# Kernel tuning notes

Hardware: AMD Instinct MI355X
Metric: run time of the kernel (lower is better)

Reference implementation:

```python
import jax, jax.numpy as jnp
import numpy as np

B, V, E, D_IN, D_OUT = 8, 10000, 160000, 128, 128
BN_EPS = 1e-5


def setup_inputs() -> dict:
    key = jax.random.key(0)
    ks = jax.random.split(key, 8)
    X = jax.random.normal(ks[0], (B, V, D_IN), dtype=jnp.float32)
    edge_attr = jax.random.normal(ks[1], (B, E), dtype=jnp.float32)
    W_node = jax.random.normal(ks[2], (D_OUT, D_IN), dtype=jnp.float32) * (1.0 / np.sqrt(D_IN))
    W_edge = jax.random.normal(ks[3], (D_OUT, 1), dtype=jnp.float32)
    W_self = jax.random.normal(ks[4], (D_OUT, D_IN), dtype=jnp.float32) * (1.0 / np.sqrt(D_IN))
    b_self = jax.random.normal(ks[5], (D_OUT,), dtype=jnp.float32) * 0.01
    gamma = jnp.ones((D_OUT,), dtype=jnp.float32)
    beta = jnp.zeros((D_OUT,), dtype=jnp.float32)
    edge_index = jax.random.randint(ks[6], (E, 2), 0, V, dtype=jnp.int32)
    return {"X": X, "edge_attr": edge_attr, "W_node": W_node, "W_edge": W_edge,
            "W_self": W_self, "b_self": b_self, "gamma": gamma, "beta": beta,
            "edge_index": edge_index}


def reference(X, edge_attr, W_node, W_edge, W_self, b_self, gamma, beta, edge_index):
    src = edge_index[:, 0]  # [E]
    dst = edge_index[:, 1]  # [E]
    # self-loop linear
    H = jnp.einsum('bvf,of->bvo', X, W_self) + b_self  # [B,V,D_OUT]
    # fused gather -> per-edge message -> scatter-add
    msg = jnp.einsum('bef,of->beo', X[:, src, :], W_node)  # [B,E,D_OUT]
    msg = msg + edge_attr[:, :, None] * W_edge[:, 0][None, None, :]
    aggregated = jnp.zeros_like(H).at[:, dst, :].add(msg)
    H = H + aggregated
    # BatchNorm1d over channel dim (training mode, biased variance over B*V)
    mean = jnp.mean(H, axis=(0, 1))
    var = jnp.var(H, axis=(0, 1))
    Hn = (H - mean) * jax.lax.rsqrt(var + BN_EPS) * gamma + beta
    return jax.nn.relu(Hn)
```

## Files before the change

### kernel.cpp

```cpp
#include <hip/hip_runtime.h>

#define B_ 8
#define V_ 10000
#define E_ 160000
#define DIN 128
#define DOUT 128
#define M_ (B_*V_)
#define NINV (1.0f/80000.0f)
#define BN_EPS 1e-5f

#define GEMM_BLOCKS 625

#define WS_COUNTS  0
#define WS_SUM     10000
#define WS_SUMSQ   10128
#define WS_ROWPTR  10512
#define WS_CURSOR  20513
#define WS_SSRC    30513
#define WS_EAS     190520
#define WS_S       1470520
#define WS_WPK     1550520
#define WS_XH      1566904
#define WS_AH      6686904
#define WS_PART    11806904
#define WS_ZERO_UNITS 10000

typedef __attribute__((ext_vector_type(2))) _Float16 half2_t;
typedef __attribute__((ext_vector_type(4))) _Float16 half4_t;
typedef __attribute__((ext_vector_type(8))) _Float16 half8_t;
typedef __attribute__((ext_vector_type(4))) float f32x4;

__device__ inline half2_t i2h(unsigned i) {
    half2_t h; __builtin_memcpy(&h, &i, 4); return h;
}
__device__ inline unsigned h2i(half2_t h) {
    unsigned i; __builtin_memcpy(&i, &h, 4); return i;
}

__global__ __launch_bounds__(256) void prep_kernel(
    const float* __restrict__ X, _Float16* __restrict__ Xh,
    const float* __restrict__ Wself, const float* __restrict__ Wnode,
    _Float16* __restrict__ Wpk,
    const int* __restrict__ EI, int* __restrict__ counts)
{
    const int blk = blockIdx.x;
    const int t = threadIdx.x;
    if (blk < 10000) {
        int idx = blk * 256 + t;
        float4 v = ((const float4*)X)[idx];
        half4_t o = { (_Float16)v.x, (_Float16)v.y, (_Float16)v.z, (_Float16)v.w };
        ((half4_t*)Xh)[idx] = o;
    } else if (blk < 10016) {
        int g = (blk - 10000) * 256 + t;
        int pair = g >> 6;
        int lane = g & 63;
        int ks = pair >> 3;
        int nt = pair & 7;
        int o = nt * 16 + (lane & 15);
        int k = ks * 32 + (lane >> 4) * 8;
        const float* wsrc = (k < 128) ? (Wself + o * 128 + k)
                                      : (Wnode + o * 128 + (k - 128));
        _Float16* dst = Wpk + ((size_t)pair * 64 + lane) * 8;
#pragma unroll
        for (int j = 0; j < 8; ++j) dst[j] = (_Float16)wsrc[j];
    } else {
        int e = (blk - 10016) * 256 + t;
        if (e < E_) atomicAdd(&counts[EI[2 * e + 1]], 1);
    }
}

__global__ __launch_bounds__(256) void scan_kernel(
    const int* __restrict__ counts, int* __restrict__ row_ptr,
    int* __restrict__ cursor)
{
    __shared__ int psum[256];
    const int t = threadIdx.x;
    const int base = t * 40;
    int local[40];
    int s = 0;
#pragma unroll
    for (int i = 0; i < 40; ++i) {
        int idx = base + i;
        int c = (idx < V_) ? counts[idx] : 0;
        local[i] = s;
        s += c;
    }
    psum[t] = s;
    __syncthreads();
    for (int off = 1; off < 256; off <<= 1) {
        int v = (t >= off) ? psum[t - off] : 0;
        __syncthreads();
        psum[t] += v;
        __syncthreads();
    }
    int excl = (t == 0) ? 0 : psum[t - 1];
#pragma unroll
    for (int i = 0; i < 40; ++i) {
        int idx = base + i;
        if (idx < V_) {
            int rp = excl + local[i];
            row_ptr[idx] = rp;
            cursor[idx] = rp;
        }
    }
    if (t == 255) row_ptr[V_] = psum[255];
}

__global__ __launch_bounds__(256) void bucket_kernel(
    const int* __restrict__ EI, const float* __restrict__ EA,
    int* __restrict__ cursor, int* __restrict__ ssrc,
    float* __restrict__ EAs)
{
    int e = blockIdx.x * 256 + threadIdx.x;
    if (e < E_) {
        int src = EI[2 * e];
        int dst = EI[2 * e + 1];
        int p = atomicAdd(&cursor[dst], 1);
        ssrc[p] = src;
        float4 v0, v1;
        v0.x = EA[0 * E_ + e]; v0.y = EA[1 * E_ + e];
        v0.z = EA[2 * E_ + e]; v0.w = EA[3 * E_ + e];
        v1.x = EA[4 * E_ + e]; v1.y = EA[5 * E_ + e];
        v1.z = EA[6 * E_ + e]; v1.w = EA[7 * E_ + e];
        *(float4*)(EAs + (size_t)p * 8) = v0;
        *(float4*)(EAs + (size_t)p * 8 + 4) = v1;
    }
}

__global__ __launch_bounds__(256) void gather_kernel(
    const _Float16* __restrict__ Xh, const float* __restrict__ EAs,
    const int* __restrict__ row_ptr, const int* __restrict__ ssrc,
    _Float16* __restrict__ Ah, float* __restrict__ S)
{
    const int b = blockIdx.x & 7;
    const int dblk = blockIdx.x >> 3;
    const int w = threadIdx.x >> 6;
    const int lane = threadIdx.x & 63;
    const int half = lane >> 5;
    const int sl = lane & 31;
    const int d = dblk * 4 + w;
    const int wid = b * V_ + d;
    const int k0 = row_ptr[d];
    const int k1 = row_ptr[d + 1];
    const _Float16* Xb = Xh + (size_t)b * V_ * DIN + sl * 4;
    half2_t a0 = (half2_t)0, a1 = (half2_t)0;
    float ea = 0.0f;
    for (int kb = k0; kb < k1; kb += 64) {
        int cnt = min(64, k1 - kb);
        int msrc = 0;
        if (lane < cnt) {
            msrc = ssrc[kb + lane];
            ea += EAs[(size_t)(kb + lane) * 8 + b];
        }
        int j = 0;
        for (; j + 8 <= cnt; j += 8) {
#pragma unroll
            for (int u = 0; u < 4; ++u) {
                int s = __shfl(msrc, j + u * 2 + half);
                uint2 v = *(const uint2*)(Xb + (size_t)s * DIN);
                a0 += i2h(v.x);
                a1 += i2h(v.y);
            }
        }
        for (; j + 2 <= cnt; j += 2) {
            int s = __shfl(msrc, j + half);
            uint2 v = *(const uint2*)(Xb + (size_t)s * DIN);
            a0 += i2h(v.x);
            a1 += i2h(v.y);
        }
        if (j < cnt) {
            int s = __shfl(msrc, j);
            if (half == 0) {
                uint2 v = *(const uint2*)(Xb + (size_t)s * DIN);
                a0 += i2h(v.x);
                a1 += i2h(v.y);
            }
        }
    }
    unsigned c0 = __shfl_down(h2i(a0), 32);
    unsigned c1 = __shfl_down(h2i(a1), 32);
    a0 += i2h(c0);
    a1 += i2h(c1);
    for (int off = 32; off; off >>= 1) ea += __shfl_down(ea, off);
    if (lane == 0) S[wid] = ea;
    if (half == 0) {
        uint2 o;
        o.x = h2i(a0);
        o.y = h2i(a1);
        *(uint2*)(Ah + (size_t)wid * DIN + sl * 4) = o;
    }
}

__global__ __launch_bounds__(256) void mfma_gemm_kernel(
    const _Float16* __restrict__ Xh, const _Float16* __restrict__ Ah,
    const _Float16* __restrict__ Wpk, const float* __restrict__ S,
    const float* __restrict__ bself, const float* __restrict__ wedge,
    float* __restrict__ H, float* __restrict__ Partials)
{
    __shared__ float cs[128];
    __shared__ float css[128];
    const int t = threadIdx.x;
    const int wave = t >> 6;
    const int lane = t & 63;
    const int quad = lane >> 4;
    const int ln = lane & 15;
    const int rowbase = blockIdx.x * 128 + wave * 32;
    const int m0 = rowbase + ln;
    const int m1 = rowbase + 16 + ln;

    if (t < 128) { cs[t] = 0.0f; css[t] = 0.0f; }

    f32x4 acc[2][8];
#pragma unroll
    for (int mt = 0; mt < 2; ++mt)
#pragma unroll
        for (int nt = 0; nt < 8; ++nt) acc[mt][nt] = (f32x4){0.f, 0.f, 0.f, 0.f};

    const _Float16* X0 = Xh + (size_t)m0 * DIN + quad * 8;
    const _Float16* X1 = Xh + (size_t)m1 * DIN + quad * 8;
    const _Float16* A0 = Ah + (size_t)m0 * DIN + quad * 8;
    const _Float16* A1 = Ah + (size_t)m1 * DIN + quad * 8;
    const _Float16* Wl = Wpk + lane * 8;

#pragma unroll
    for (int ks = 0; ks < 8; ++ks) {
        half8_t af0, af1;
        if (ks < 4) {
            af0 = *(const half8_t*)(X0 + ks * 32);
            af1 = *(const half8_t*)(X1 + ks * 32);
        } else {
            af0 = *(const half8_t*)(A0 + (ks - 4) * 32);
            af1 = *(const half8_t*)(A1 + (ks - 4) * 32);
        }
#pragma unroll
        for (int nt = 0; nt < 8; ++nt) {
            half8_t bfr = *(const half8_t*)(Wl + (size_t)(ks * 8 + nt) * 512);
            acc[0][nt] = __builtin_amdgcn_mfma_f32_16x16x32_f16(af0, bfr, acc[0][nt], 0, 0, 0);
            acc[1][nt] = __builtin_amdgcn_mfma_f32_16x16x32_f16(af1, bfr, acc[1][nt], 0, 0, 0);
        }
    }

    float bs[8], we[8];
#pragma unroll
    for (int nt = 0; nt < 8; ++nt) {
        int c = nt * 16 + ln;
        bs[nt] = bself[c];
        we[nt] = wedge[c];
    }
    float psum[8], psq[8];
#pragma unroll
    for (int nt = 0; nt < 8; ++nt) { psum[nt] = 0.0f; psq[nt] = 0.0f; }

#pragma unroll
    for (int mt = 0; mt < 2; ++mt) {
        const int rbase = rowbase + mt * 16 + quad * 4;
        float sv[4];
#pragma unroll
        for (int r = 0; r < 4; ++r) sv[r] = S[rbase + r];
#pragma unroll
        for (int r = 0; r < 4; ++r) {
            float* Hr = H + (size_t)(rbase + r) * DOUT + ln;
#pragma unroll
            for (int nt = 0; nt < 8; ++nt) {
                float h = acc[mt][nt][r] + bs[nt] + sv[r] * we[nt];
                Hr[nt * 16] = h;
                psum[nt] += h;
                psq[nt] += h * h;
            }
        }
    }
#pragma unroll
    for (int nt = 0; nt < 8; ++nt) {
        psum[nt] += __shfl_down(psum[nt], 32);
        psum[nt] += __shfl_down(psum[nt], 16);
        psq[nt] += __shfl_down(psq[nt], 32);
        psq[nt] += __shfl_down(psq[nt], 16);
    }
    __syncthreads();
    if (lane < 16) {
#pragma unroll
        for (int nt = 0; nt < 8; ++nt) {
            atomicAdd(&cs[nt * 16 + ln], psum[nt]);
            atomicAdd(&css[nt * 16 + ln], psq[nt]);
        }
    }
    __syncthreads();
    Partials[(size_t)blockIdx.x * 256 + t] = (t < 128) ? cs[t] : css[t - 128];
}

__global__ __launch_bounds__(64) void reduce_stats_kernel(
    const float* __restrict__ Partials, float* __restrict__ gsum,
    float* __restrict__ gsumsq)
{
    const int c = blockIdx.x;
    const int t = threadIdx.x;
    float acc = 0.0f;
    for (int p = t; p < GEMM_BLOCKS; p += 64)
        acc += Partials[(size_t)p * 256 + c];
    for (int off = 32; off; off >>= 1) acc += __shfl_down(acc, off);
    if (t == 0) {
        if (c < 128) gsum[c] = acc;
        else gsumsq[c - 128] = acc;
    }
}

__global__ __launch_bounds__(256) void norm_relu_kernel(
    float* __restrict__ H, const float* __restrict__ gsum,
    const float* __restrict__ gsumsq, const float* __restrict__ gamma,
    const float* __restrict__ beta)
{
    int idx = blockIdx.x * 256 + threadIdx.x;
    int o4 = (idx & 31) * 4;
    float4 s = *(const float4*)(gsum + o4);
    float4 q = *(const float4*)(gsumsq + o4);
    float4 g = *(const float4*)(gamma + o4);
    float4 bt = *(const float4*)(beta + o4);
    float4 sc, sh;
    {
        float m0 = s.x * NINV, m1 = s.y * NINV, m2 = s.z * NINV, m3 = s.w * NINV;
        float r0 = rsqrtf(q.x * NINV - m0 * m0 + BN_EPS);
        float r1 = rsqrtf(q.y * NINV - m1 * m1 + BN_EPS);
        float r2 = rsqrtf(q.z * NINV - m2 * m2 + BN_EPS);
        float r3 = rsqrtf(q.w * NINV - m3 * m3 + BN_EPS);
        sc.x = g.x * r0; sc.y = g.y * r1; sc.z = g.z * r2; sc.w = g.w * r3;
        sh.x = bt.x - m0 * sc.x; sh.y = bt.y - m1 * sc.y;
        sh.z = bt.z - m2 * sc.z; sh.w = bt.w - m3 * sc.w;
    }
    float4 h = ((const float4*)H)[idx];
    h.x = fmaxf(h.x * sc.x + sh.x, 0.0f);
    h.y = fmaxf(h.y * sc.y + sh.y, 0.0f);
    h.z = fmaxf(h.z * sc.z + sh.z, 0.0f);
    h.w = fmaxf(h.w * sc.w + sh.w, 0.0f);
    ((float4*)H)[idx] = h;
}

extern "C" void kernel_launch(void* const* d_in, const int* in_sizes, int n_in,
                              void* d_out, int out_size, void* d_ws, size_t ws_size,
                              hipStream_t stream)
{
    const float* X      = (const float*)d_in[0];
    const float* EA     = (const float*)d_in[1];
    const float* Wnode  = (const float*)d_in[2];
    const float* Wedge  = (const float*)d_in[3];
    const float* Wself  = (const float*)d_in[4];
    const float* bself  = (const float*)d_in[5];
    const float* gamma  = (const float*)d_in[6];
    const float* beta   = (const float*)d_in[7];
    const int*   EI     = (const int*)d_in[8];

    int*   wsI    = (int*)d_ws;
    float* wsF    = (float*)d_ws;
    int*   counts = wsI + WS_COUNTS;
    float* gsum   = wsF + WS_SUM;
    float* gsumsq = wsF + WS_SUMSQ;
    int*   rowptr = wsI + WS_ROWPTR;
    int*   cursor = wsI + WS_CURSOR;
    int*   ssrc   = wsI + WS_SSRC;
    float* EAs    = wsF + WS_EAS;
    float* S      = wsF + WS_S;
    _Float16* Wpk = (_Float16*)(wsI + WS_WPK);
    _Float16* Xh  = (_Float16*)(wsI + WS_XH);
    _Float16* Ah  = (_Float16*)(wsI + WS_AH);
    float* Partials = wsF + WS_PART;
    float* H      = (float*)d_out;

    hipMemsetAsync(d_ws, 0, (size_t)WS_ZERO_UNITS * 4, stream);

    prep_kernel<<<10641, 256, 0, stream>>>(X, Xh, Wself, Wnode, Wpk, EI, counts);
    scan_kernel<<<1, 256, 0, stream>>>(counts, rowptr, cursor);
    bucket_kernel<<<(E_ + 255) / 256, 256, 0, stream>>>(EI, EA, cursor, ssrc, EAs);

    gather_kernel<<<M_ / 4, 256, 0, stream>>>(Xh, EAs, rowptr, ssrc, Ah, S);

    mfma_gemm_kernel<<<GEMM_BLOCKS, 256, 0, stream>>>(Xh, Ah, Wpk, S, bself,
                                                      Wedge, H, Partials);

    reduce_stats_kernel<<<256, 64, 0, stream>>>(Partials, gsum, gsumsq);

    norm_relu_kernel<<<(M_ * DOUT / 4) / 256, 256, 0, stream>>>(H, gsum, gsumsq,
                                                                gamma, beta);
}
```

Measured before the change: 226.3 us.

## Fuse GEMM, BN stats reduction and norm-ReLU into cooperative kernel; widen gather loads

```diff
diff --git a/kernel.cpp b/kernel.cpp
--- a/kernel.cpp
+++ b/kernel.cpp
@@ -1,4 +1,7 @@
 #include <hip/hip_runtime.h>
+#include <hip/hip_cooperative_groups.h>
+
+namespace cg = cooperative_groups;
 
 #define B_ 8
 #define V_ 10000
@@ -136,14 +139,14 @@
     const int dblk = blockIdx.x >> 3;
     const int w = threadIdx.x >> 6;
     const int lane = threadIdx.x & 63;
-    const int half = lane >> 5;
-    const int sl = lane & 31;
+    const int q = lane >> 4;
+    const int sl = lane & 15;
     const int d = dblk * 4 + w;
     const int wid = b * V_ + d;
     const int k0 = row_ptr[d];
     const int k1 = row_ptr[d + 1];
-    const _Float16* Xb = Xh + (size_t)b * V_ * DIN + sl * 4;
-    half2_t a0 = (half2_t)0, a1 = (half2_t)0;
+    const _Float16* Xb = Xh + (size_t)b * V_ * DIN + sl * 8;
+    half2_t a0 = (half2_t)0, a1 = (half2_t)0, a2 = (half2_t)0, a3 = (half2_t)0;
     float ea = 0.0f;
     for (int kb = k0; kb < k1; kb += 64) {
         int cnt = min(64, k1 - kb);
@@ -153,64 +156,59 @@
             ea += EAs[(size_t)(kb + lane) * 8 + b];
         }
         int j = 0;
-        for (; j + 8 <= cnt; j += 8) {
+        for (; j + 16 <= cnt; j += 16) {
 #pragma unroll
             for (int u = 0; u < 4; ++u) {
-                int s = __shfl(msrc, j + u * 2 + half);
-                uint2 v = *(const uint2*)(Xb + (size_t)s * DIN);
-                a0 += i2h(v.x);
-                a1 += i2h(v.y);
+                int s = __shfl(msrc, j + u * 4 + q);
+                uint4 v = *(const uint4*)(Xb + (size_t)s * DIN);
+                a0 += i2h(v.x); a1 += i2h(v.y); a2 += i2h(v.z); a3 += i2h(v.w);
             }
         }
-        for (; j + 2 <= cnt; j += 2) {
-            int s = __shfl(msrc, j + half);
-            uint2 v = *(const uint2*)(Xb + (size_t)s * DIN);
-            a0 += i2h(v.x);
-            a1 += i2h(v.y);
+        for (; j + 4 <= cnt; j += 4) {
+            int s = __shfl(msrc, j + q);
+            uint4 v = *(const uint4*)(Xb + (size_t)s * DIN);
+            a0 += i2h(v.x); a1 += i2h(v.y); a2 += i2h(v.z); a3 += i2h(v.w);
         }
         if (j < cnt) {
-            int s = __shfl(msrc, j);
-            if (half == 0) {
-                uint2 v = *(const uint2*)(Xb + (size_t)s * DIN);
-                a0 += i2h(v.x);
-                a1 += i2h(v.y);
+            int s = __shfl(msrc, j + q);
+            if (j + q < cnt) {
+                uint4 v = *(const uint4*)(Xb + (size_t)s * DIN);
+                a0 += i2h(v.x); a1 += i2h(v.y); a2 += i2h(v.z); a3 += i2h(v.w);
             }
         }
     }
-    unsigned c0 = __shfl_down(h2i(a0), 32);
-    unsigned c1 = __shfl_down(h2i(a1), 32);
-    a0 += i2h(c0);
-    a1 += i2h(c1);
+#pragma unroll
+    for (int off = 32; off >= 16; off >>= 1) {
+        a0 += i2h(__shfl_down(h2i(a0), off));
+        a1 += i2h(__shfl_down(h2i(a1), off));
+        a2 += i2h(__shfl_down(h2i(a2), off));
+        a3 += i2h(__shfl_down(h2i(a3), off));
+    }
     for (int off = 32; off; off >>= 1) ea += __shfl_down(ea, off);
     if (lane == 0) S[wid] = ea;
-    if (half == 0) {
-        uint2 o;
-        o.x = h2i(a0);
-        o.y = h2i(a1);
-        *(uint2*)(Ah + (size_t)wid * DIN + sl * 4) = o;
-    }
-}
-
-__global__ __launch_bounds__(256) void mfma_gemm_kernel(
+    if (lane < 16) {
+        uint4 o;
+        o.x = h2i(a0); o.y = h2i(a1); o.z = h2i(a2); o.w = h2i(a3);
+        *(uint4*)(Ah + (size_t)wid * DIN + sl * 8) = o;
+    }
+}
+
+__device__ __forceinline__ void gemm_body(
     const _Float16* __restrict__ Xh, const _Float16* __restrict__ Ah,
     const _Float16* __restrict__ Wpk, const float* __restrict__ S,
     const float* __restrict__ bself, const float* __restrict__ wedge,
-    float* __restrict__ H, float* __restrict__ Partials)
-{
-    __shared__ float cs[128];
-    __shared__ float css[128];
-    const int t = threadIdx.x;
+    int bid, int t, f32x4 (&acc)[2][8], float* cs, float* css)
+{
     const int wave = t >> 6;
     const int lane = t & 63;
     const int quad = lane >> 4;
     const int ln = lane & 15;
-    const int rowbase = blockIdx.x * 128 + wave * 32;
+    const int rowbase = bid * 128 + wave * 32;
     const int m0 = rowbase + ln;
     const int m1 = rowbase + 16 + ln;
 
     if (t < 128) { cs[t] = 0.0f; css[t] = 0.0f; }
 
-    f32x4 acc[2][8];
 #pragma unroll
     for (int mt = 0; mt < 2; ++mt)
 #pragma unroll
@@ -258,12 +256,11 @@
 #pragma unroll
         for (int r = 0; r < 4; ++r) sv[r] = S[rbase + r];
 #pragma unroll
-        for (int r = 0; r < 4; ++r) {
-            float* Hr = H + (size_t)(rbase + r) * DOUT + ln;
-#pragma unroll
-            for (int nt = 0; nt < 8; ++nt) {
+        for (int nt = 0; nt < 8; ++nt) {
+#pragma unroll
+            for (int r = 0; r < 4; ++r) {
                 float h = acc[mt][nt][r] + bs[nt] + sv[r] * we[nt];
-                Hr[nt * 16] = h;
+                acc[mt][nt][r] = h;
                 psum[nt] += h;
                 psq[nt] += h * h;
             }
@@ -285,6 +282,99 @@
         }
     }
     __syncthreads();
+}
+
+__global__ __launch_bounds__(256, 4) void gemm_norm_coop_kernel(
+    const _Float16* __restrict__ Xh, const _Float16* __restrict__ Ah,
+    const _Float16* __restrict__ Wpk, const float* __restrict__ S,
+    const float* __restrict__ bself, const float* __restrict__ wedge,
+    const float* __restrict__ gamma, const float* __restrict__ beta,
+    float* __restrict__ H, float* __restrict__ Partials,
+    float* __restrict__ gsum, float* __restrict__ gsumsq)
+{
+    __shared__ float cs[128];
+    __shared__ float css[128];
+    const int t = threadIdx.x;
+    f32x4 acc[2][8];
+    gemm_body(Xh, Ah, Wpk, S, bself, wedge, blockIdx.x, t, acc, cs, css);
+
+    Partials[(size_t)blockIdx.x * 256 + t] = (t < 128) ? cs[t] : css[t - 128];
+    __threadfence();
+    cg::this_grid().sync();
+
+    if (blockIdx.x < 256 && t < 64) {
+        const int c = blockIdx.x;
+        float a = 0.0f;
+        for (int p = t; p < GEMM_BLOCKS; p += 64)
+            a += Partials[(size_t)p * 256 + c];
+        for (int off = 32; off; off >>= 1) a += __shfl_down(a, off);
+        if (t == 0) {
+            if (c < 128) gsum[c] = a;
+            else gsumsq[c - 128] = a;
+        }
+        __threadfence();
+    }
+    cg::this_grid().sync();
+
+    const int wave = t >> 6;
+    const int lane = t & 63;
+    const int quad = lane >> 4;
+    const int ln = lane & 15;
+    const int rowbase = blockIdx.x * 128 + wave * 32;
+    float scl[8], shf[8];
+#pragma unroll
+    for (int nt = 0; nt < 8; ++nt) {
+        int c = nt * 16 + ln;
+        float gs = __hip_atomic_load(&gsum[c], __ATOMIC_RELAXED,
+                                     __HIP_MEMORY_SCOPE_AGENT);
+        float gq = __hip_atomic_load(&gsumsq[c], __ATOMIC_RELAXED,
+                                     __HIP_MEMORY_SCOPE_AGENT);
+        float mean = gs * NINV;
+        float rstd = rsqrtf(gq * NINV - mean * mean + BN_EPS);
+        scl[nt] = gamma[c] * rstd;
+        shf[nt] = beta[c] - mean * scl[nt];
+    }
+#pragma unroll
+    for (int mt = 0; mt < 2; ++mt) {
+        const int rbase = rowbase + mt * 16 + quad * 4;
+#pragma unroll
+        for (int r = 0; r < 4; ++r) {
+            float* Hr = H + (size_t)(rbase + r) * DOUT + ln;
+#pragma unroll
+            for (int nt = 0; nt < 8; ++nt)
+                Hr[nt * 16] = fmaxf(acc[mt][nt][r] * scl[nt] + shf[nt], 0.0f);
+        }
+    }
+}
+
+__global__ __launch_bounds__(256) void mfma_gemm_kernel(
+    const _Float16* __restrict__ Xh, const _Float16* __restrict__ Ah,
+    const _Float16* __restrict__ Wpk, const float* __restrict__ S,
+    const float* __restrict__ bself, const float* __restrict__ wedge,
+    float* __restrict__ H, float* __restrict__ Partials)
+{
+    __shared__ float cs[128];
+    __shared__ float css[128];
+    const int t = threadIdx.x;
+    f32x4 acc[2][8];
+    gemm_body(Xh, Ah, Wpk, S, bself, wedge, blockIdx.x, t, acc, cs, css);
+
+    const int wave = t >> 6;
+    const int lane = t & 63;
+    const int quad = lane >> 4;
+    const int ln = lane & 15;
+    const int rowbase = blockIdx.x * 128 + wave * 32;
+#pragma unroll
+    for (int mt = 0; mt < 2; ++mt) {
+        const int rbase = rowbase + mt * 16 + quad * 4;
+#pragma unroll
+        for (int r = 0; r < 4; ++r) {
+            float* Hr = H + (size_t)(rbase + r) * DOUT + ln;
+#pragma unroll
+            for (int nt = 0; nt < 8; ++nt)
+                Hr[nt * 16] = acc[mt][nt][r];
+        }
+    }
     Partials[(size_t)blockIdx.x * 256 + t] = (t < 128) ? cs[t] : css[t - 128];
 }
 
@@ -372,11 +462,23 @@
 
     gather_kernel<<<M_ / 4, 256, 0, stream>>>(Xh, EAs, rowptr, ssrc, Ah, S);
 
+    int blocksPerCU = 0;
+    hipError_t qerr = hipOccupancyMaxActiveBlocksPerMultiprocessor(
+        &blocksPerCU, gemm_norm_coop_kernel, 256, 0);
+    bool coop = (qerr == hipSuccess) && (blocksPerCU * 256 >= GEMM_BLOCKS);
+    if (coop) {
+        void* args[] = { (void*)&Xh, (void*)&Ah, (void*)&Wpk, (void*)&S,
+                         (void*)&bself, (void*)&Wedge, (void*)&gamma,
+                         (void*)&beta, (void*)&H, (void*)&Partials,
+                         (void*)&gsum, (void*)&gsumsq };
+        hipError_t lerr = hipLaunchCooperativeKernel(
+            (void*)gemm_norm_coop_kernel, dim3(GEMM_BLOCKS), dim3(256),
+            args, 0, stream);
+        if (lerr == hipSuccess) return;
+    }
     mfma_gemm_kernel<<<GEMM_BLOCKS, 256, 0, stream>>>(Xh, Ah, Wpk, S, bself,
                                                       Wedge, H, Partials);
-
     reduce_stats_kernel<<<256, 64, 0, stream>>>(Partials, gsum, gsumsq);
-
     norm_relu_kernel<<<(M_ * DOUT / 4) / 256, 256, 0, stream>>>(H, gsum, gsumsq,
                                                                 gamma, beta);
 }
```

After: 221.6 us. -2.1%, faster.
